# Optimization experiments

Measured on AMD Instinct MI355X. Metric: run time of the kernel, lower is better.

## Reference

```python
import jax, jax.numpy as jnp
import numpy as np

N = 50000          # num nodes
E = 800000         # num edges (before self loops)
DIM_IN = 128
HID = 32           # per-head hidden of conv1
HEADS = 8          # heads of conv1
DIM_OUT = 16       # output classes (conv2, 1 head, concat=False)
NEG_SLOPE = 0.2    # GATConv default leaky_relu slope


def gat_conv(x, W, a_src, a_dst, bias, src, dst, heads, out_ch, concat):
    """PyG GATConv (self-loops already appended to src/dst).
    x: [N, F_in], W: [F_in, heads*out_ch], a_src/a_dst: [heads, out_ch], bias matches output.
    """
    n = x.shape[0]
    h = (x @ W).reshape(n, heads, out_ch)                    # [N, H, C]
    al_src = jnp.einsum('nhc,hc->nh', h, a_src)              # [N, H]
    al_dst = jnp.einsum('nhc,hc->nh', h, a_dst)              # [N, H]
    e = jax.nn.leaky_relu(al_src[src] + al_dst[dst], NEG_SLOPE)   # [E', H]
    # segment softmax over edges grouped by target node (dst)
    emax = jax.ops.segment_max(e, dst, num_segments=n)       # [N, H]
    ee = jnp.exp(e - emax[dst])                              # [E', H]
    denom = jax.ops.segment_sum(ee, dst, num_segments=n)     # [N, H]
    alpha = ee / (denom[dst] + 1e-16)                        # [E', H]
    msg = h[src] * alpha[:, :, None]                         # [E', H, C]
    out = jax.ops.segment_sum(msg, dst, num_segments=n)      # [N, H, C]
    out = out.reshape(n, heads * out_ch) if concat else out.mean(axis=1)
    return out + bias


def setup_inputs() -> dict:
    key = jax.random.key(0)
    ks = jax.random.split(key, 12)
    x = jax.random.normal(ks[0], (N, DIM_IN), dtype=jnp.float32)
    edge_index = jax.random.randint(ks[1], (2, E), 0, N, dtype=jnp.int64)
    s = 0.1
    W1 = jax.random.normal(ks[2], (DIM_IN, HEADS * HID), dtype=jnp.float32) * s
    a1_src = jax.random.normal(ks[3], (HEADS, HID), dtype=jnp.float32) * s
    a1_dst = jax.random.normal(ks[4], (HEADS, HID), dtype=jnp.float32) * s
    b1 = jnp.zeros((HEADS * HID,), dtype=jnp.float32)
    W2 = jax.random.normal(ks[5], (HEADS * HID, DIM_OUT), dtype=jnp.float32) * s
    a2_src = jax.random.normal(ks[6], (1, DIM_OUT), dtype=jnp.float32) * s
    a2_dst = jax.random.normal(ks[7], (1, DIM_OUT), dtype=jnp.float32) * s
    b2 = jnp.zeros((DIM_OUT,), dtype=jnp.float32)
    return {"x": x, "edge_index": edge_index, "W1": W1, "a1_src": a1_src,
            "a1_dst": a1_dst, "b1": b1, "W2": W2, "a2_src": a2_src,
            "a2_dst": a2_dst, "b2": b2}


def reference(x, edge_index, W1, a1_src, a1_dst, b1, W2, a2_src, a2_dst, b2):
    # add self loops (GATConv default add_self_loops=True)
    loops = jnp.arange(N, dtype=edge_index.dtype)
    src = jnp.concatenate([edge_index[0], loops])
    dst = jnp.concatenate([edge_index[1], loops])
    # dropout layers are identity in eval mode
    h = gat_conv(x, W1, a1_src, a1_dst, b1, src, dst, HEADS, HID, concat=True)
    h = jax.nn.elu(h)
    out = gat_conv(h, W2, a2_src, a2_dst, b2, src, dst, 1, DIM_OUT, concat=False)
    return jax.nn.log_softmax(out, axis=1)
```

## Files before the change

### kernel.cpp

```cpp
#include <hip/hip_runtime.h>
#include <hip/hip_bf16.h>

#define NN 50000
#define EE 800000
#define EP (EE + NN)
#define DIN 128
#define HID 32
#define HEADS 8
#define C1 (HEADS * HID)
#define DOUT 16
#define NW1 3125
#define SH 8
#define NB 196
#define CAP 8192
#define EPT 8
#define BBLK (256 * EPT)
#define GB ((NW1 * 64 + 255) / 256)
#define BB ((EP + BBLK - 1) / BBLK)

typedef __attribute__((ext_vector_type(8))) short short8;
typedef __attribute__((ext_vector_type(4))) float float4v;
typedef __attribute__((ext_vector_type(2))) float float2v;

__device__ inline unsigned short f2bf(float f) {
    __hip_bfloat16 b = __float2bfloat16(f);
    return *reinterpret_cast<unsigned short*>(&b);
}
__device__ inline float bflo(unsigned u) {
    union { unsigned int i; float f; } x;
    x.i = u << 16;
    return x.f;
}
__device__ inline float bfhi(unsigned u) {
    union { unsigned int i; float f; } x;
    x.i = u & 0xffff0000u;
    return x.f;
}
__device__ inline float bf2f(unsigned short u) {
    union { unsigned int i; float f; } x;
    x.i = ((unsigned int)u) << 16;
    return x.f;
}

__global__ void k_prepfw(const float* __restrict__ W1, const float* __restrict__ a1s,
                         const float* __restrict__ a1d, const float* __restrict__ W2,
                         unsigned short* __restrict__ w1frag,
                         unsigned short* __restrict__ w2frag,
                         int* __restrict__ cntb) {
    int i = blockIdx.x * 256 + threadIdx.x;
    if (blockIdx.x == 0 && threadIdx.x < NB) cntb[threadIdx.x] = 0;
    if (i < 17 * 2048) {
        int j = i & 7, lane = (i >> 3) & 63, s = (i >> 9) & 3, c = i >> 11;
        int q = lane >> 4, m = lane & 15;
        int k = s * 32 + q * 8 + j;
        float val;
        if (c < 16) {
            val = W1[k * C1 + c * 16 + m];
        } else {
            int h = m & 7;
            const float* av = (m < 8) ? a1s : a1d;
            float acc = 0.f;
            #pragma unroll
            for (int j2 = 0; j2 < 32; j2++)
                acc += W1[k * C1 + h * 32 + j2] * av[h * 32 + j2];
            val = acc;
        }
        w1frag[i] = f2bf(val);
    } else if (i < 17 * 2048 + 8 * 512) {
        int j2 = i - 17 * 2048;
        int jj = j2 & 7, lane = (j2 >> 3) & 63, s = j2 >> 9;
        int q = lane >> 4, m = lane & 15;
        w2frag[j2] = f2bf(W2[(s * 32 + q * 8 + jj) * DOUT + m]);
    }
}

__global__ __launch_bounds__(256) void k_g1bkt(const float* __restrict__ x,
                                               const unsigned short* __restrict__ w1frag,
                                               unsigned char* __restrict__ h1f8,
                                               float* __restrict__ al1sd,
                                               unsigned short* __restrict__ al1s8,
                                               const int* __restrict__ ei,
                                               int* __restrict__ cntb,
                                               unsigned* __restrict__ ebuf) {
    __shared__ int hist[4][NB];
    __shared__ int base[4][NB];
    int bid = blockIdx.x;
    if (bid < GB) {
        int wid = (bid * 256 + threadIdx.x) >> 6;
        int lane = threadIdx.x & 63;
        if (wid >= NW1) return;
        int nb = wid * 16;
        int m = lane & 15, quad = lane >> 4;
        const float* xrow = x + (nb + m) * DIN;

        float4 xf[8];
        #pragma unroll
        for (int s = 0; s < 4; s++) {
            xf[2 * s]     = *(const float4*)(xrow + s * 32 + quad * 8);
            xf[2 * s + 1] = *(const float4*)(xrow + s * 32 + quad * 8 + 4);
        }
        short8 bfr[4];
        #pragma unroll
        for (int s = 0; s < 4; s++) {
            unsigned short* bp = (unsigned short*)&bfr[s];
            float4 f0 = xf[2 * s], f1 = xf[2 * s + 1];
            bp[0] = f2bf(f0.x); bp[1] = f2bf(f0.y); bp[2] = f2bf(f0.z); bp[3] = f2bf(f0.w);
            bp[4] = f2bf(f1.x); bp[5] = f2bf(f1.y); bp[6] = f2bf(f1.z); bp[7] = f2bf(f1.w);
        }

        float4v acc[17];
        #pragma unroll
        for (int c = 0; c < 17; c++) acc[c] = (float4v){0.f, 0.f, 0.f, 0.f};

        #pragma unroll
        for (int s = 0; s < 4; s++) {
            const unsigned short* fp = w1frag + (s * 64 + lane) * 8;
            #pragma unroll
            for (int c = 0; c < 17; c++) {
                short8 afrag = *(const short8*)(fp + c * 2048);
                acc[c] = __builtin_amdgcn_mfma_f32_16x16x32_bf16(afrag, bfr[s], acc[c], 0, 0, 0);
            }
        }

        int node = nb + m;
        #pragma unroll
        for (int c = 0; c < 16; c++) {
            unsigned pk = 0;
            pk = __builtin_amdgcn_cvt_pk_fp8_f32(acc[c][0], acc[c][1], pk, false);
            pk = __builtin_amdgcn_cvt_pk_fp8_f32(acc[c][2], acc[c][3], pk, true);
            *(unsigned*)(h1f8 + node * C1 + c * 16 + quad * 4) = pk;
        }
        *(float4*)(al1sd + node * 16 + quad * 4) =
            make_float4(acc[16][0], acc[16][1], acc[16][2], acc[16][3]);
        if (quad < 2) {
            uint2 pk;
            pk.x = (unsigned)f2bf(acc[16][0]) | ((unsigned)f2bf(acc[16][1]) << 16);
            pk.y = (unsigned)f2bf(acc[16][2]) | ((unsigned)f2bf(acc[16][3]) << 16);
            *(uint2*)(al1s8 + node * 8 + quad * 4) = pk;
        }
    } else {
        int t = threadIdx.x;
        int wave = t >> 6;
        for (int i = t; i < 4 * NB; i += 256) ((int*)hist)[i] = 0;
        __syncthreads();
        int e0 = (bid - GB) * BBLK;
        int s[EPT], d[EPT], r[EPT];
        #pragma unroll
        for (int j = 0; j < EPT; j++) {
            int e = e0 + j * 256 + t;
            int ss = 0, dd = -1;
            if (e < EE) { ss = ei[e]; dd = ei[EE + e]; }
            else if (e < EP) { ss = e - EE; dd = ss; }
            s[j] = ss; d[j] = dd;
            if (dd >= 0) r[j] = atomicAdd(&hist[wave][dd >> SH], 1);
        }
        __syncthreads();
        if (t < NB) {
            int h0 = hist[0][t], h1 = hist[1][t], h2 = hist[2][t], h3 = hist[3][t];
            int tot = h0 + h1 + h2 + h3;
            int bb = tot ? atomicAdd(&cntb[t], tot) : 0;
            base[0][t] = bb;
            base[1][t] = bb + h0;
            base[2][t] = bb + h0 + h1;
            base[3][t] = bb + h0 + h1 + h2;
        }
        __syncthreads();
        #pragma unroll
        for (int j = 0; j < EPT; j++) {
            if (d[j] >= 0) {
                int b = d[j] >> SH;
                ebuf[b * CAP + base[wave][b] + r[j]] =
                    ((unsigned)s[j] << SH) | (unsigned)(d[j] & 255);
            }
        }
    }
}

__global__ __launch_bounds__(1024) void k_csr(const int* __restrict__ cntb,
                                              const unsigned* __restrict__ ebuf,
                                              int* __restrict__ row_ptr,
                                              int* __restrict__ esrc) {
    __shared__ int sdeg[256];
    __shared__ int wtot[4];
    __shared__ int bpart[4];
    int b = blockIdx.x;
    int t = threadIdx.x;
    int lane = t & 63, wave = t >> 6;
    int nodes0 = b << SH;
    if (t < 256) sdeg[t] = 0;
    if (t < 256) {
        int v = (t < b) ? cntb[t] : 0;
        #pragma unroll
        for (int off = 1; off < 64; off <<= 1) v += __shfl_xor(v, off, 64);
        if (lane == 0) bpart[wave] = v;
    }
    __syncthreads();
    int baseS = bpart[0] + bpart[1] + bpart[2] + bpart[3];
    int cnt = cntb[b];
    const unsigned* eb = ebuf + b * CAP;
    for (int i = t; i < cnt; i += 1024)
        atomicAdd(&sdeg[eb[i] & 255], 1);
    __syncthreads();
    int v = (t < 256) ? sdeg[t] : 0;
    int inc = v;
    #pragma unroll
    for (int off = 1; off < 64; off <<= 1) {
        int u = __shfl_up(inc, off, 64);
        if (lane >= off) inc += u;
    }
    if (t < 256 && lane == 63) wtot[wave] = inc;
    __syncthreads();
    if (wave == 0 && lane < 4) {
        int w = wtot[lane];
        int iw = w;
        #pragma unroll
        for (int off = 1; off < 4; off <<= 1) {
            int u = __shfl_up(iw, off, 64);
            if (lane >= off) iw += u;
        }
        wtot[lane] = iw - w;
    }
    __syncthreads();
    int excl = inc - v + ((t < 256) ? wtot[wave] : 0);
    __syncthreads();
    if (t < 256) {
        sdeg[t] = excl;
        int node = nodes0 + t;
        if (node < NN) row_ptr[node] = baseS + excl;
    }
    __syncthreads();
    for (int i = t; i < cnt; i += 1024) {
        unsigned e = eb[i];
        int pos = atomicAdd(&sdeg[e & 255], 1);
        esrc[baseS + pos] = (int)(e >> SH);
    }
    if (b == 0 && t == 0) row_ptr[NN] = EP;
}

__global__ __launch_bounds__(256) void k_agg1(const int* __restrict__ row_ptr,
                                              const int* __restrict__ esrc,
                                              const unsigned char* __restrict__ h1f8,
                                              const unsigned short* __restrict__ al1s8,
                                              const float* __restrict__ al1sd,
                                              const float* __restrict__ b1,
                                              unsigned short* __restrict__ helu_b) {
    __shared__ float wbuf[4][64 * 8];
    __shared__ int   sbuf[4][64];
    int wslot = threadIdx.x >> 6;
    int L = threadIdx.x & 63;
    int d = (blockIdx.x * 256 + threadIdx.x) >> 6;
    int h = L >> 3;
    int start = row_ptr[d], end = row_ptr[d + 1];
    float4 ald0 = *(const float4*)(al1sd + d * 16 + 8);
    float4 ald1 = *(const float4*)(al1sd + d * 16 + 12);
    float* wrow = wbuf[wslot];
    int* srow = sbuf[wslot];
    float denom = 0.f;
    float4 acc = make_float4(0.f, 0.f, 0.f, 0.f);
    const int Lofs = L * 4;

    for (int base = start; base < end; base += 64) {
        int cnt = min(64, end - base);
        int s = d;
        float wv0 = 0.f, wv1 = 0.f, wv2 = 0.f, wv3 = 0.f;
        float wv4 = 0.f, wv5 = 0.f, wv6 = 0.f, wv7 = 0.f;
        if (L < cnt) {
            s = esrc[base + L];
            uint4 as = *(const uint4*)(al1s8 + s * 8);
            float e;
            e = bflo(as.x) + ald0.x; e = e > 0.f ? e : 0.2f * e; wv0 = __expf(e);
            e = bfhi(as.x) + ald0.y; e = e > 0.f ? e : 0.2f * e; wv1 = __expf(e);
            e = bflo(as.y) + ald0.z; e = e > 0.f ? e : 0.2f * e; wv2 = __expf(e);
            e = bfhi(as.y) + ald0.w; e = e > 0.f ? e : 0.2f * e; wv3 = __expf(e);
            e = bflo(as.z) + ald1.x; e = e > 0.f ? e : 0.2f * e; wv4 = __expf(e);
            e = bfhi(as.z) + ald1.y; e = e > 0.f ? e : 0.2f * e; wv5 = __expf(e);
            e = bflo(as.w) + ald1.z; e = e > 0.f ? e : 0.2f * e; wv6 = __expf(e);
            e = bfhi(as.w) + ald1.w; e = e > 0.f ? e : 0.2f * e; wv7 = __expf(e);
        }
        srow[L] = s;
        *(float4*)&wrow[L * 8]     = make_float4(wv0, wv1, wv2, wv3);
        *(float4*)&wrow[L * 8 + 4] = make_float4(wv4, wv5, wv6, wv7);
        int cnt8 = (cnt + 7) & ~7;
        for (int i = 0; i < cnt8; i += 8) {
            unsigned v[8];
            float xw[8];
            #pragma unroll
            for (int j = 0; j < 8; j++) {
                int sj = srow[i + j];
                xw[j] = wrow[(i + j) * 8 + h];
                v[j] = *(const unsigned*)(h1f8 + sj * C1 + Lofs);
            }
            #pragma unroll
            for (int j = 0; j < 8; j++) {
                float2v a = __builtin_amdgcn_cvt_pk_f32_fp8(v[j], false);
                float2v b = __builtin_amdgcn_cvt_pk_f32_fp8(v[j], true);
                float xj = xw[j];
                denom += xj;
                acc.x += xj * a.x; acc.y += xj * a.y; acc.z += xj * b.x; acc.w += xj * b.y;
            }
        }
    }
    float inv = 1.0f / (denom + 1e-16f);
    float4 bv = *(const float4*)(b1 + Lofs);
    float o0 = acc.x * inv + bv.x;
    float o1 = acc.y * inv + bv.y;
    float o2 = acc.z * inv + bv.z;
    float o3 = acc.w * inv + bv.w;
    o0 = o0 > 0.f ? o0 : __expf(o0) - 1.0f;
    o1 = o1 > 0.f ? o1 : __expf(o1) - 1.0f;
    o2 = o2 > 0.f ? o2 : __expf(o2) - 1.0f;
    o3 = o3 > 0.f ? o3 : __expf(o3) - 1.0f;
    uint2 pk;
    pk.x = (unsigned)f2bf(o0) | ((unsigned)f2bf(o1) << 16);
    pk.y = (unsigned)f2bf(o2) | ((unsigned)f2bf(o3) << 16);
    *(uint2*)(helu_b + d * C1 + Lofs) = pk;
}

__global__ __launch_bounds__(256) void k_gemm2(const unsigned short* __restrict__ helu_b,
                                               const unsigned short* __restrict__ w2frag,
                                               const float* __restrict__ a2s,
                                               const float* __restrict__ a2d,
                                               unsigned short* __restrict__ h2b,
                                               float* __restrict__ al2s,
                                               float* __restrict__ al2d) {
    int wid = (blockIdx.x * 256 + threadIdx.x) >> 6;
    int lane = threadIdx.x & 63;
    int nb = wid * 16;
    if (nb >= NN) return;
    int m = lane & 15, quad = lane >> 4;

    const unsigned short* wp2 = w2frag + lane * 8;
    float4v acc = {0.f, 0.f, 0.f, 0.f};
    const unsigned short* arow = helu_b + (nb + m) * C1 + quad * 8;
    #pragma unroll
    for (int s = 0; s < 8; s++) {
        short8 afrag = *(const short8*)(arow + s * 32);
        short8 bfrag = *(const short8*)(wp2 + s * 512);
        acc = __builtin_amdgcn_mfma_f32_16x16x32_bf16(afrag, bfrag, acc, 0, 0, 0);
    }

    float as_c = a2s[m], ad_c = a2d[m];
    #pragma unroll
    for (int r = 0; r < 4; r++) {
        int node = nb + quad * 4 + r;
        float val = acc[r];
        h2b[node * DOUT + m] = f2bf(val);
        float ps = val * as_c;
        float pd = val * ad_c;
        ps += __shfl_xor(ps, 1, 64); ps += __shfl_xor(ps, 2, 64);
        ps += __shfl_xor(ps, 4, 64); ps += __shfl_xor(ps, 8, 64);
        pd += __shfl_xor(pd, 1, 64); pd += __shfl_xor(pd, 2, 64);
        pd += __shfl_xor(pd, 4, 64); pd += __shfl_xor(pd, 8, 64);
        if (m == 0) {
            al2s[node] = ps;
            al2d[node] = pd;
        }
    }
}

__global__ __launch_bounds__(256) void k_agg2(const int* __restrict__ row_ptr,
                                              const int* __restrict__ esrc,
                                              const unsigned short* __restrict__ h2b,
                                              const float* __restrict__ al2s,
                                              const float* __restrict__ al2d,
                                              const float* __restrict__ b2,
                                              float* __restrict__ out) {
    __shared__ float wbuf2[4][64];
    __shared__ int   sbuf2[4][64];
    int wslot = threadIdx.x >> 6;
    int L = threadIdx.x & 63;
    int n = (blockIdx.x * 256 + threadIdx.x) >> 6;
    if (n >= NN) return;
    int p = L & 7, g = L >> 3;
    int start = row_ptr[n], end = row_ptr[n + 1];
    float ald = al2d[n];
    float* wrow = wbuf2[wslot];
    int* srow = sbuf2[wslot];
    float acc0 = 0.f, acc1 = 0.f, denom = 0.f;

    for (int base = start; base < end; base += 64) {
        int cnt = min(64, end - base);
        int s = n; float w = 0.f;
        if (L < cnt) {
            s = esrc[base + L];
            float e = al2s[s] + ald;
            e = e > 0.f ? e : 0.2f * e;
            w = __expf(e);
        }
        srow[L] = s;
        wrow[L] = w;
        int cnt8 = (cnt + 7) & ~7;
        for (int i = 0; i < cnt8; i += 8) {
            int idx = i + g;
            int ss = srow[idx];
            float ww = wrow[idx];
            unsigned v = *(const unsigned*)(h2b + ss * DOUT + p * 2);
            acc0 += ww * bflo(v);
            acc1 += ww * bfhi(v);
            denom += ww;
        }
    }
    acc0 += __shfl_xor(acc0, 8, 64);  acc0 += __shfl_xor(acc0, 16, 64);  acc0 += __shfl_xor(acc0, 32, 64);
    acc1 += __shfl_xor(acc1, 8, 64);  acc1 += __shfl_xor(acc1, 16, 64);  acc1 += __shfl_xor(acc1, 32, 64);
    denom += __shfl_xor(denom, 8, 64); denom += __shfl_xor(denom, 16, 64); denom += __shfl_xor(denom, 32, 64);
    float inv = 1.0f / (denom + 1e-16f);
    float2 bv = *(const float2*)(b2 + p * 2);
    float val0 = acc0 * inv + bv.x;
    float val1 = acc1 * inv + bv.y;
    float m = fmaxf(val0, val1);
    #pragma unroll
    for (int mm = 1; mm < 8; mm <<= 1) m = fmaxf(m, __shfl_xor(m, mm, 64));
    float se = __expf(val0 - m) + __expf(val1 - m);
    #pragma unroll
    for (int mm = 1; mm < 8; mm <<= 1) se += __shfl_xor(se, mm, 64);
    float lse = m + __logf(se);
    if (L < 8) {
        float2 o = make_float2(val0 - lse, val1 - lse);
        *(float2*)(out + n * DOUT + p * 2) = o;
    }
}

extern "C" void kernel_launch(void* const* d_in, const int* in_sizes, int n_in,
                              void* d_out, int out_size, void* d_ws, size_t ws_size,
                              hipStream_t stream) {
    const float* x   = (const float*)d_in[0];
    const int*   ei  = (const int*)d_in[1];
    const float* W1  = (const float*)d_in[2];
    const float* a1s = (const float*)d_in[3];
    const float* a1d = (const float*)d_in[4];
    const float* b1  = (const float*)d_in[5];
    const float* W2  = (const float*)d_in[6];
    const float* a2s = (const float*)d_in[7];
    const float* a2d = (const float*)d_in[8];
    const float* b2  = (const float*)d_in[9];
    float* outp = (float*)d_out;

    unsigned char* h1f8    = (unsigned char*)d_ws;
    unsigned short* helu_b = (unsigned short*)(h1f8 + NN * C1);
    unsigned short* h2b    = helu_b + NN * C1;
    unsigned short* w2frag = h2b + NN * DOUT;
    unsigned short* w1frag = w2frag + 8 * 512;
    unsigned short* al1s8  = w1frag + 17 * 2048;
    float* al1sd = (float*)(al1s8 + NN * 8);
    float* al2sb = al1sd + NN * 16;
    float* al2db = al2sb + NN;
    int* row_ptr = (int*)(al2db + NN);
    int* esrc    = row_ptr + NN + 1;
    int* cntb    = esrc + EP;
    unsigned* ebuf = (unsigned*)helu_b;

    k_prepfw<<<(17 * 2048 + 8 * 512 + 255) / 256, 256, 0, stream>>>(W1, a1s, a1d, W2, w1frag, w2frag, cntb);
    k_g1bkt<<<GB + BB, 256, 0, stream>>>(x, w1frag, h1f8, al1sd, al1s8, ei, cntb, ebuf);
    k_csr<<<NB, 1024, 0, stream>>>(cntb, ebuf, row_ptr, esrc);
    k_agg1<<<12500, 256, 0, stream>>>(row_ptr, esrc, h1f8, al1s8, al1sd, b1, helu_b);
    k_gemm2<<<(NW1 * 64 + 255) / 256, 256, 0, stream>>>(helu_b, w2frag, a2s, a2d, h2b, al2sb, al2db);
    k_agg2<<<(NN * 64 + 255) / 256, 256, 0, stream>>>(row_ptr, esrc, h2b, al2sb, al2db, b2, outp);
}
```

Baseline: 200.8 us.

## Precompute per-edge attention weights in CSR build and stream them into aggregation

Moves the layer-1 per-edge leaky-relu and exp computation out of k_agg1 and into the CSR scatter loop of k_csr. That loop writes 8 fp32 weights per edge into a new wedge buffer in CSR order, which removes the bf16 al1s8 side buffer. k_agg1 now reads the weights sequentially, stores them head-major in padded shared memory, and gets source indices by readlane from a register instead of from shared memory. The cost is an extra 850K×32-byte write and read of wedge, and k_csr, which runs as only 196 blocks, now does gathered al1sd loads and exps.

```diff
diff --git a/kernel.cpp b/kernel.cpp
--- a/kernel.cpp
+++ b/kernel.cpp
@@ -34,11 +34,6 @@
 __device__ inline float bfhi(unsigned u) {
     union { unsigned int i; float f; } x;
     x.i = u & 0xffff0000u;
-    return x.f;
-}
-__device__ inline float bf2f(unsigned short u) {
-    union { unsigned int i; float f; } x;
-    x.i = ((unsigned int)u) << 16;
     return x.f;
 }
 
@@ -78,7 +73,6 @@
                                                const unsigned short* __restrict__ w1frag,
                                                unsigned char* __restrict__ h1f8,
                                                float* __restrict__ al1sd,
-                                               unsigned short* __restrict__ al1s8,
                                                const int* __restrict__ ei,
                                                int* __restrict__ cntb,
                                                unsigned* __restrict__ ebuf) {
@@ -132,12 +126,6 @@
         }
         *(float4*)(al1sd + node * 16 + quad * 4) =
             make_float4(acc[16][0], acc[16][1], acc[16][2], acc[16][3]);
-        if (quad < 2) {
-            uint2 pk;
-            pk.x = (unsigned)f2bf(acc[16][0]) | ((unsigned)f2bf(acc[16][1]) << 16);
-            pk.y = (unsigned)f2bf(acc[16][2]) | ((unsigned)f2bf(acc[16][3]) << 16);
-            *(uint2*)(al1s8 + node * 8 + quad * 4) = pk;
-        }
     } else {
         int t = threadIdx.x;
         int wave = t >> 6;
@@ -178,8 +166,10 @@
 
 __global__ __launch_bounds__(1024) void k_csr(const int* __restrict__ cntb,
                                               const unsigned* __restrict__ ebuf,
+                                              const float* __restrict__ al1sd,
                                               int* __restrict__ row_ptr,
-                                              int* __restrict__ esrc) {
+                                              int* __restrict__ esrc,
+                                              float* __restrict__ wedge) {
     __shared__ int sdeg[256];
     __shared__ int wtot[4];
     __shared__ int bpart[4];
@@ -231,64 +221,77 @@
     __syncthreads();
     for (int i = t; i < cnt; i += 1024) {
         unsigned e = eb[i];
-        int pos = atomicAdd(&sdeg[e & 255], 1);
-        esrc[baseS + pos] = (int)(e >> SH);
+        int dloc = (int)(e & 255);
+        int src = (int)(e >> SH);
+        int dst = nodes0 + dloc;
+        int pos = atomicAdd(&sdeg[dloc], 1);
+        int g = baseS + pos;
+        esrc[g] = src;
+        float4 ls0 = *(const float4*)(al1sd + src * 16);
+        float4 ls1 = *(const float4*)(al1sd + src * 16 + 4);
+        float4 ld0 = *(const float4*)(al1sd + dst * 16 + 8);
+        float4 ld1 = *(const float4*)(al1sd + dst * 16 + 12);
+        float ee0, ee1, ee2, ee3, ee4, ee5, ee6, ee7;
+        ee0 = ls0.x + ld0.x; ee0 = ee0 > 0.f ? ee0 : 0.2f * ee0;
+        ee1 = ls0.y + ld0.y; ee1 = ee1 > 0.f ? ee1 : 0.2f * ee1;
+        ee2 = ls0.z + ld0.z; ee2 = ee2 > 0.f ? ee2 : 0.2f * ee2;
+        ee3 = ls0.w + ld0.w; ee3 = ee3 > 0.f ? ee3 : 0.2f * ee3;
+        ee4 = ls1.x + ld1.x; ee4 = ee4 > 0.f ? ee4 : 0.2f * ee4;
+        ee5 = ls1.y + ld1.y; ee5 = ee5 > 0.f ? ee5 : 0.2f * ee5;
+        ee6 = ls1.z + ld1.z; ee6 = ee6 > 0.f ? ee6 : 0.2f * ee6;
+        ee7 = ls1.w + ld1.w; ee7 = ee7 > 0.f ? ee7 : 0.2f * ee7;
+        *(float4*)(wedge + g * 8) =
+            make_float4(__expf(ee0), __expf(ee1), __expf(ee2), __expf(ee3));
+        *(float4*)(wedge + g * 8 + 4) =
+            make_float4(__expf(ee4), __expf(ee5), __expf(ee6), __expf(ee7));
     }
     if (b == 0 && t == 0) row_ptr[NN] = EP;
 }
 
 __global__ __launch_bounds__(256) void k_agg1(const int* __restrict__ row_ptr,
                                               const int* __restrict__ esrc,
+                                              const float* __restrict__ wedge,
                                               const unsigned char* __restrict__ h1f8,
-                                              const unsigned short* __restrict__ al1s8,
-                                              const float* __restrict__ al1sd,
                                               const float* __restrict__ b1,
                                               unsigned short* __restrict__ helu_b) {
-    __shared__ float wbuf[4][64 * 8];
-    __shared__ int   sbuf[4][64];
+    __shared__ float wbuf[4][8 * 68];
     int wslot = threadIdx.x >> 6;
     int L = threadIdx.x & 63;
-    int d = (blockIdx.x * 256 + threadIdx.x) >> 6;
-    int h = L >> 3;
+    int d = __builtin_amdgcn_readfirstlane((int)((blockIdx.x * 256 + threadIdx.x) >> 6));
     int start = row_ptr[d], end = row_ptr[d + 1];
-    float4 ald0 = *(const float4*)(al1sd + d * 16 + 8);
-    float4 ald1 = *(const float4*)(al1sd + d * 16 + 12);
     float* wrow = wbuf[wslot];
-    int* srow = sbuf[wslot];
+    const int hbase = (L >> 3) * 68;
+    const int Lofs = L * 4;
     float denom = 0.f;
     float4 acc = make_float4(0.f, 0.f, 0.f, 0.f);
-    const int Lofs = L * 4;
 
     for (int base = start; base < end; base += 64) {
         int cnt = min(64, end - base);
-        int s = d;
-        float wv0 = 0.f, wv1 = 0.f, wv2 = 0.f, wv3 = 0.f;
-        float wv4 = 0.f, wv5 = 0.f, wv6 = 0.f, wv7 = 0.f;
+        int sval = d;
+        float4 w0 = make_float4(0.f, 0.f, 0.f, 0.f);
+        float4 w1 = make_float4(0.f, 0.f, 0.f, 0.f);
         if (L < cnt) {
-            s = esrc[base + L];
-            uint4 as = *(const uint4*)(al1s8 + s * 8);
-            float e;
-            e = bflo(as.x) + ald0.x; e = e > 0.f ? e : 0.2f * e; wv0 = __expf(e);
-            e = bfhi(as.x) + ald0.y; e = e > 0.f ? e : 0.2f * e; wv1 = __expf(e);
-            e = bflo(as.y) + ald0.z; e = e > 0.f ? e : 0.2f * e; wv2 = __expf(e);
-            e = bfhi(as.y) + ald0.w; e = e > 0.f ? e : 0.2f * e; wv3 = __expf(e);
-            e = bflo(as.z) + ald1.x; e = e > 0.f ? e : 0.2f * e; wv4 = __expf(e);
-            e = bfhi(as.z) + ald1.y; e = e > 0.f ? e : 0.2f * e; wv5 = __expf(e);
-            e = bflo(as.w) + ald1.z; e = e > 0.f ? e : 0.2f * e; wv6 = __expf(e);
-            e = bfhi(as.w) + ald1.w; e = e > 0.f ? e : 0.2f * e; wv7 = __expf(e);
-        }
-        srow[L] = s;
-        *(float4*)&wrow[L * 8]     = make_float4(wv0, wv1, wv2, wv3);
-        *(float4*)&wrow[L * 8 + 4] = make_float4(wv4, wv5, wv6, wv7);
+            sval = esrc[base + L];
+            w0 = *(const float4*)(wedge + (size_t)(base + L) * 8);
+            w1 = *(const float4*)(wedge + (size_t)(base + L) * 8 + 4);
+        }
+        wrow[0 * 68 + L] = w0.x;
+        wrow[1 * 68 + L] = w0.y;
+        wrow[2 * 68 + L] = w0.z;
+        wrow[3 * 68 + L] = w0.w;
+        wrow[4 * 68 + L] = w1.x;
+        wrow[5 * 68 + L] = w1.y;
+        wrow[6 * 68 + L] = w1.z;
+        wrow[7 * 68 + L] = w1.w;
         int cnt8 = (cnt + 7) & ~7;
         for (int i = 0; i < cnt8; i += 8) {
             unsigned v[8];
             float xw[8];
             #pragma unroll
             for (int j = 0; j < 8; j++) {
-                int sj = srow[i + j];
-                xw[j] = wrow[(i + j) * 8 + h];
+                int sj = __builtin_amdgcn_readlane(sval, i + j);
                 v[j] = *(const unsigned*)(h1f8 + sj * C1 + Lofs);
+                xw[j] = wrow[hbase + i + j];
             }
             #pragma unroll
             for (int j = 0; j < 8; j++) {
@@ -440,19 +443,19 @@
     unsigned short* h2b    = helu_b + NN * C1;
     unsigned short* w2frag = h2b + NN * DOUT;
     unsigned short* w1frag = w2frag + 8 * 512;
-    unsigned short* al1s8  = w1frag + 17 * 2048;
-    float* al1sd = (float*)(al1s8 + NN * 8);
+    float* al1sd = (float*)(w1frag + 17 * 2048);
     float* al2sb = al1sd + NN * 16;
     float* al2db = al2sb + NN;
     int* row_ptr = (int*)(al2db + NN);
     int* esrc    = row_ptr + NN + 1;
     int* cntb    = esrc + EP;
+    float* wedge = (float*)(cntb + NB + 64);
     unsigned* ebuf = (unsigned*)helu_b;
 
     k_prepfw<<<(17 * 2048 + 8 * 512 + 255) / 256, 256, 0, stream>>>(W1, a1s, a1d, W2, w1frag, w2frag, cntb);
-    k_g1bkt<<<GB + BB, 256, 0, stream>>>(x, w1frag, h1f8, al1sd, al1s8, ei, cntb, ebuf);
-    k_csr<<<NB, 1024, 0, stream>>>(cntb, ebuf, row_ptr, esrc);
-    k_agg1<<<12500, 256, 0, stream>>>(row_ptr, esrc, h1f8, al1s8, al1sd, b1, helu_b);
+    k_g1bkt<<<GB + BB, 256, 0, stream>>>(x, w1frag, h1f8, al1sd, ei, cntb, ebuf);
+    k_csr<<<NB, 1024, 0, stream>>>(cntb, ebuf, al1sd, row_ptr, esrc, wedge);
+    k_agg1<<<12500, 256, 0, stream>>>(row_ptr, esrc, wedge, h1f8, b1, helu_b);
     k_gemm2<<<(NW1 * 64 + 255) / 256, 256, 0, stream>>>(helu_b, w2frag, a2s, a2d, h2b, al2sb, al2db);
     k_agg2<<<(NN * 64 + 255) / 256, 256, 0, stream>>>(row_ptr, esrc, h2b, al2sb, al2db, b2, outp);
 }
```

Result: slower. 214.2 us (+6.7%).

## Compute edge attention weights per 8-edge group with wave shuffles instead of LDS

Applied to the files above, without the earlier changes.

The layer-1 aggregation no longer has each lane compute all 8 head weights for one edge and stage them through shared memory. Each group of 8 lanes now handles one edge, one head per lane, reading the fp32 source logit directly, and the weights reach the consuming lanes through cross-lane shuffles. Source indices are broadcast with readlane, and the bf16 copy of the source logits is no longer written. This removes LDS traffic, the extra bf16 buffer write and redundant exp work on padding lanes. In exchange it adds a shuffle per edge and scattered 4-byte gathers of al1sd per inner step.

```diff
diff --git a/kernel.cpp b/kernel.cpp
--- a/kernel.cpp
+++ b/kernel.cpp
@@ -34,11 +34,6 @@
 __device__ inline float bfhi(unsigned u) {
     union { unsigned int i; float f; } x;
     x.i = u & 0xffff0000u;
-    return x.f;
-}
-__device__ inline float bf2f(unsigned short u) {
-    union { unsigned int i; float f; } x;
-    x.i = ((unsigned int)u) << 16;
     return x.f;
 }
 
@@ -78,7 +73,6 @@
                                                const unsigned short* __restrict__ w1frag,
                                                unsigned char* __restrict__ h1f8,
                                                float* __restrict__ al1sd,
-                                               unsigned short* __restrict__ al1s8,
                                                const int* __restrict__ ei,
                                                int* __restrict__ cntb,
                                                unsigned* __restrict__ ebuf) {
@@ -132,12 +126,6 @@
         }
         *(float4*)(al1sd + node * 16 + quad * 4) =
             make_float4(acc[16][0], acc[16][1], acc[16][2], acc[16][3]);
-        if (quad < 2) {
-            uint2 pk;
-            pk.x = (unsigned)f2bf(acc[16][0]) | ((unsigned)f2bf(acc[16][1]) << 16);
-            pk.y = (unsigned)f2bf(acc[16][2]) | ((unsigned)f2bf(acc[16][3]) << 16);
-            *(uint2*)(al1s8 + node * 8 + quad * 4) = pk;
-        }
     } else {
         int t = threadIdx.x;
         int wave = t >> 6;
@@ -239,56 +227,39 @@
 
 __global__ __launch_bounds__(256) void k_agg1(const int* __restrict__ row_ptr,
                                               const int* __restrict__ esrc,
+                                              const float* __restrict__ al1sd,
                                               const unsigned char* __restrict__ h1f8,
-                                              const unsigned short* __restrict__ al1s8,
-                                              const float* __restrict__ al1sd,
                                               const float* __restrict__ b1,
                                               unsigned short* __restrict__ helu_b) {
-    __shared__ float wbuf[4][64 * 8];
-    __shared__ int   sbuf[4][64];
-    int wslot = threadIdx.x >> 6;
     int L = threadIdx.x & 63;
-    int d = (blockIdx.x * 256 + threadIdx.x) >> 6;
-    int h = L >> 3;
+    int d = __builtin_amdgcn_readfirstlane((int)((blockIdx.x * 256 + threadIdx.x) >> 6));
     int start = row_ptr[d], end = row_ptr[d + 1];
-    float4 ald0 = *(const float4*)(al1sd + d * 16 + 8);
-    float4 ald1 = *(const float4*)(al1sd + d * 16 + 12);
-    float* wrow = wbuf[wslot];
-    int* srow = sbuf[wslot];
+    const int Lofs = L * 4;
+    const int hprod = L & 7;
+    const int hcons = L >> 3;
+    float ald_p = al1sd[d * 16 + 8 + hprod];
     float denom = 0.f;
     float4 acc = make_float4(0.f, 0.f, 0.f, 0.f);
-    const int Lofs = L * 4;
 
     for (int base = start; base < end; base += 64) {
         int cnt = min(64, end - base);
-        int s = d;
-        float wv0 = 0.f, wv1 = 0.f, wv2 = 0.f, wv3 = 0.f;
-        float wv4 = 0.f, wv5 = 0.f, wv6 = 0.f, wv7 = 0.f;
-        if (L < cnt) {
-            s = esrc[base + L];
-            uint4 as = *(const uint4*)(al1s8 + s * 8);
-            float e;
-            e = bflo(as.x) + ald0.x; e = e > 0.f ? e : 0.2f * e; wv0 = __expf(e);
-            e = bfhi(as.x) + ald0.y; e = e > 0.f ? e : 0.2f * e; wv1 = __expf(e);
-            e = bflo(as.y) + ald0.z; e = e > 0.f ? e : 0.2f * e; wv2 = __expf(e);
-            e = bfhi(as.y) + ald0.w; e = e > 0.f ? e : 0.2f * e; wv3 = __expf(e);
-            e = bflo(as.z) + ald1.x; e = e > 0.f ? e : 0.2f * e; wv4 = __expf(e);
-            e = bfhi(as.z) + ald1.y; e = e > 0.f ? e : 0.2f * e; wv5 = __expf(e);
-            e = bflo(as.w) + ald1.z; e = e > 0.f ? e : 0.2f * e; wv6 = __expf(e);
-            e = bfhi(as.w) + ald1.w; e = e > 0.f ? e : 0.2f * e; wv7 = __expf(e);
-        }
-        srow[L] = s;
-        *(float4*)&wrow[L * 8]     = make_float4(wv0, wv1, wv2, wv3);
-        *(float4*)&wrow[L * 8 + 4] = make_float4(wv4, wv5, wv6, wv7);
+        int sval = d;
+        if (L < cnt) sval = esrc[base + L];
         int cnt8 = (cnt + 7) & ~7;
         for (int i = 0; i < cnt8; i += 8) {
+            int eidx = i + (L >> 3);
+            int sp = __shfl(sval, eidx, 64);
+            float as = al1sd[sp * 16 + hprod];
+            float e = as + ald_p;
+            e = e > 0.f ? e : 0.2f * e;
+            float w = (eidx < cnt) ? __expf(e) : 0.f;
             unsigned v[8];
             float xw[8];
             #pragma unroll
             for (int j = 0; j < 8; j++) {
-                int sj = srow[i + j];
-                xw[j] = wrow[(i + j) * 8 + h];
+                int sj = __builtin_amdgcn_readlane(sval, i + j);
                 v[j] = *(const unsigned*)(h1f8 + sj * C1 + Lofs);
+                xw[j] = __shfl(w, j * 8 + hcons, 64);
             }
             #pragma unroll
             for (int j = 0; j < 8; j++) {
@@ -440,8 +411,7 @@
     unsigned short* h2b    = helu_b + NN * C1;
     unsigned short* w2frag = h2b + NN * DOUT;
     unsigned short* w1frag = w2frag + 8 * 512;
-    unsigned short* al1s8  = w1frag + 17 * 2048;
-    float* al1sd = (float*)(al1s8 + NN * 8);
+    float* al1sd = (float*)(w1frag + 17 * 2048);
     float* al2sb = al1sd + NN * 16;
     float* al2db = al2sb + NN;
     int* row_ptr = (int*)(al2db + NN);
@@ -450,9 +420,9 @@
     unsigned* ebuf = (unsigned*)helu_b;
 
     k_prepfw<<<(17 * 2048 + 8 * 512 + 255) / 256, 256, 0, stream>>>(W1, a1s, a1d, W2, w1frag, w2frag, cntb);
-    k_g1bkt<<<GB + BB, 256, 0, stream>>>(x, w1frag, h1f8, al1sd, al1s8, ei, cntb, ebuf);
+    k_g1bkt<<<GB + BB, 256, 0, stream>>>(x, w1frag, h1f8, al1sd, ei, cntb, ebuf);
     k_csr<<<NB, 1024, 0, stream>>>(cntb, ebuf, row_ptr, esrc);
-    k_agg1<<<12500, 256, 0, stream>>>(row_ptr, esrc, h1f8, al1s8, al1sd, b1, helu_b);
+    k_agg1<<<12500, 256, 0, stream>>>(row_ptr, esrc, al1sd, h1f8, b1, helu_b);
     k_gemm2<<<(NW1 * 64 + 255) / 256, 256, 0, stream>>>(helu_b, w2frag, a2s, a2d, h2b, al2sb, al2db);
     k_agg2<<<(NN * 64 + 255) / 256, 256, 0, stream>>>(row_ptr, esrc, h2b, al2sb, al2db, b2, outp);
 }
```

Result: no change. 198.8 us (-1.0%).
